# Performance work log

Hardware: AMD Instinct MI355X
Metric: run time of the kernel (lower is better)

The kernel has to match this reference:

```python
import jax, jax.numpy as jnp
import numpy as np

N_POS = 1024
ALPHA = 0.3
B, S = 32, 1024


def setup_inputs() -> dict:
    key = jax.random.key(0)
    k1, k2, k3, k4 = jax.random.split(key, 4)
    s_arc = jax.random.normal(k1, (B, S, S), dtype=jnp.float32)
    a_arc = jax.random.normal(k2, (B, S, S), dtype=jnp.float32)
    adds = jax.random.randint(k3, (B, S), 0, N_POS, dtype=jnp.int32)
    pos = jax.random.randint(k4, (B, S), 0, N_POS, dtype=jnp.int32)
    return {"s_arc": s_arc, "a_arc": a_arc, "adds": adds, "pos": pos}


def reference(s_arc, a_arc, adds, pos):
    n_bins = N_POS * N_POS
    # --- histogram (scatter-add) of a_arc by POS-pair index ---
    # original: _add[b,p1,p2] = adds[b,p1]*seq_len + adds[b,p2]
    sl = adds.shape[1]
    pair_idx = adds[:, :, None] * sl + adds[:, None, :]            # [B,S,S]
    # indices >= n_bins never match any bin in the original masked-sum loop;
    # segment_sum with num_segments=n_bins drops them identically.
    hist = jax.ops.segment_sum(a_arc.reshape(-1), pair_idx.reshape(-1),
                               num_segments=n_bins)                # [n_pos^2]
    score_arc = jax.nn.sigmoid(hist)
    # --- gather score back into s_arc ---
    slp = pos.shape[1]
    pidx = pos[:, :, None] * slp + pos[:, None, :]                  # [B,S,S]
    valid = pidx < n_bins
    gathered = score_arc[jnp.clip(pidx, 0, n_bins - 1)]
    return s_arc + ALPHA * jnp.where(valid, gathered, jnp.float32(0))
```

## Files before the change

### kernel.cpp

```cpp
#include <hip/hip_runtime.h>

#define NPOS 1024
#define BB   32
#define SS   1024
#define ALPHA_C 0.3f
#define CAP  128
#define PAD  1024
#define OCAP 1024
#define MAXO 16
#define PADPAIR 0x04000400u

typedef const __attribute__((address_space(1))) unsigned int guint;
typedef __attribute__((address_space(3))) unsigned int luint;

__global__ __launch_bounds__(256) void zero_fill(float4* __restrict__ p) {
    p[blockIdx.x * 256 + threadIdx.x] = make_float4(0.f, 0.f, 0.f, 0.f);
}

__global__ __launch_bounds__(1024) void build_tables(
    const int* __restrict__ adds, int* __restrict__ cnt, int* __restrict__ list,
    ushort* __restrict__ ell16, int* __restrict__ ocnt, int* __restrict__ oent) {
    __shared__ int scnt[NPOS];
    __shared__ int so;
    const int b = blockIdx.x, t = threadIdx.x;
    const int c = adds[b * SS + t];
    ((uint2*)ell16)[b * 1024 + t] = make_uint2(PADPAIR, PADPAIR);
    scnt[t] = 0;
    if (t == 0) so = 0;
    __syncthreads();
    const int rslot = atomicAdd(&cnt[c], 1);
    if (rslot < CAP) list[c * CAP + rslot] = b * SS + t;
    const int slot = atomicAdd(&scnt[c], 1);
    if (slot < 4) {
        ell16[(((size_t)b * 512 + (c & 511)) * 2 + (c >> 9)) * 4 + slot] = (ushort)t;
    } else {
        const int o = atomicAdd(&so, 1);
        if (o < OCAP) oent[b * OCAP + o] = (c << 10) | t;
    }
    __syncthreads();
    if (t == 0) ocnt[b] = (so < OCAP) ? so : OCAP;
}

__global__ __launch_bounds__(256) void overflow_fixup(
    const float* __restrict__ a, const int* __restrict__ adds,
    const int* __restrict__ ocnt, const int* __restrict__ oent,
    float* __restrict__ hist) {
    const int b  = blockIdx.x;
    const int ei = blockIdx.y;
    if (ei >= ocnt[b]) return;
    const int e  = oent[b * OCAP + ei];
    const int c  = e >> 10, p2 = e & 1023;
    const int p1 = blockIdx.z * 256 + threadIdx.x;
    const int r  = adds[b * SS + p1];
    const float v = a[((size_t)(b * SS + p1)) * SS + p2];
    atomicAdd(&hist[(size_t)r * NPOS + c], v);
}

__global__ __launch_bounds__(512) void hist_rows_kernel(
    const float* __restrict__ a, const int* __restrict__ rowcnt,
    const int* __restrict__ rowlist, const ushort* __restrict__ ell16,
    float* __restrict__ hist) {
    __shared__ float buf[2][NPOS + 2];
    __shared__ int   lsrc[CAP];
    const int r = blockIdx.x, t = threadIdx.x;
    const int w = t >> 6, lane = t & 63;

    int n = rowcnt[r]; if (n > CAP) n = CAP;
    if (t < CAP && t < n) lsrc[t] = rowlist[r * CAP + t];
    if (t == 0) { buf[0][PAD] = 0.f; buf[1][PAD] = 0.f; }
    __syncthreads();

    const uint4* ellv = (const uint4*)ell16;
    float acc0 = 0.f, acc1 = 0.f;
    uint4 E = make_uint4(PADPAIR, PADPAIR, PADPAIR, PADPAIR);

    if (n > 0) {
        if (w < 4) {
            guint* gp = (guint*)(a + (size_t)lsrc[0] * SS + (w << 8) + (lane << 2));
            luint* lp = (luint*)(void*)&buf[0][w << 8];
            __builtin_amdgcn_global_load_lds(gp, lp, 16, 0, 0);
        }
        E = ellv[(size_t)(lsrc[0] >> 10) * 512 + t];
        asm volatile("s_waitcnt vmcnt(0)" ::: "memory");
    }
    __syncthreads();

    for (int k = 0; k < n; ++k) {
        if (k + 1 < n && w < 4) {
            guint* gp = (guint*)(a + (size_t)lsrc[k + 1] * SS + (w << 8) + (lane << 2));
            luint* lp = (luint*)(void*)&buf[(k + 1) & 1][w << 8];
            __builtin_amdgcn_global_load_lds(gp, lp, 16, 0, 0);
        }
        uint4 F = make_uint4(PADPAIR, PADPAIR, PADPAIR, PADPAIR);
        if (k + 1 < n) F = ellv[(size_t)(lsrc[k + 1] >> 10) * 512 + t];

        const float* rb = buf[k & 1];
        acc0 += rb[E.x & 0xffffu]; acc0 += rb[E.x >> 16];
        acc0 += rb[E.y & 0xffffu]; acc0 += rb[E.y >> 16];
        acc1 += rb[E.z & 0xffffu]; acc1 += rb[E.z >> 16];
        acc1 += rb[E.w & 0xffffu]; acc1 += rb[E.w >> 16];
        E = F;

        asm volatile("s_waitcnt vmcnt(0) lgkmcnt(0)" ::: "memory");
        __builtin_amdgcn_s_barrier();
    }

    const size_t o0 = (size_t)r * NPOS + t;
    const float base0 = hist[o0], base1 = hist[o0 + 512];
    hist[o0]       = 1.f / (1.f + __expf(-(base0 + acc0)));
    hist[o0 + 512] = 1.f / (1.f + __expf(-(base1 + acc1)));
}

__global__ __launch_bounds__(256) void gather_kernel(
    const float* __restrict__ s, const int* __restrict__ pos,
    const float* __restrict__ score, float* __restrict__ out) {
    const int row = blockIdx.x;
    const int b   = row >> 10;
    const int*  posb = pos + b * SS;
    const int   base = posb[row & 1023] * NPOS;
    const size_t off = (size_t)row * SS;

    const int t = threadIdx.x;
    float4 v = ((const float4*)(s + off))[t];
    int4   c = ((const int4*)posb)[t];
    float4 o;
    o.x = v.x + ALPHA_C * score[base + c.x];
    o.y = v.y + ALPHA_C * score[base + c.y];
    o.z = v.z + ALPHA_C * score[base + c.z];
    o.w = v.w + ALPHA_C * score[base + c.w];
    ((float4*)(out + off))[t] = o;
}

extern "C" void kernel_launch(void* const* d_in, const int* in_sizes, int n_in,
                              void* d_out, int out_size, void* d_ws, size_t ws_size,
                              hipStream_t stream) {
    const float* s_arc = (const float*)d_in[0];
    const float* a_arc = (const float*)d_in[1];
    const int*   adds  = (const int*)d_in[2];
    const int*   pos   = (const int*)d_in[3];
    float* out  = (float*)d_out;

    float*  hist  = (float*)d_ws;
    int*    cnt   = (int*)((char*)d_ws + (size_t)NPOS * NPOS * sizeof(float));
    int*    list  = cnt + NPOS;
    ushort* ell16 = (ushort*)(list + NPOS * CAP);
    int*    ocnt  = (int*)(ell16 + (size_t)BB * NPOS * 4);
    int*    oent  = ocnt + BB;

    zero_fill<<<1025, 256, 0, stream>>>((float4*)hist);
    build_tables<<<BB, 1024, 0, stream>>>(adds, cnt, list, ell16, ocnt, oent);
    overflow_fixup<<<dim3(BB, MAXO, SS / 256), 256, 0, stream>>>(a_arc, adds, ocnt, oent, hist);
    hist_rows_kernel<<<NPOS, 512, 0, stream>>>(a_arc, cnt, list, ell16, hist);
    gather_kernel<<<BB * SS, 256, 0, stream>>>(s_arc, pos, hist, out);
}
```

Measured before the change: 138.6 us.

## Triple-buffer histogram row loads with prefetch distance two and byte-offset indices

The histogram row kernel moves from a double-buffered LDS ring to a triple-buffered one. Each source row of a_arc is prefetched two iterations ahead, and the per-iteration wait is relaxed from vmcnt(0) to vmcnt(2), so global-to-LDS loads overlap more of the gather-accumulate work. The ELL table now stores byte offsets (t<<2), which drops the index scaling from the inner loop, and the buffer stride is padded. The risk is correctness: the relaxed wait counts and the lack of an explicit lgkmcnt wait depend on the exact order in which loads are issued.

```diff
diff --git a/kernel.cpp b/kernel.cpp
--- a/kernel.cpp
+++ b/kernel.cpp
@@ -5,10 +5,10 @@
 #define SS   1024
 #define ALPHA_C 0.3f
 #define CAP  128
-#define PAD  1024
 #define OCAP 1024
 #define MAXO 16
-#define PADPAIR 0x04000400u
+#define PADPAIR 0x10001000u
+#define BSTRIDE 1032
 
 typedef const __attribute__((address_space(1))) unsigned int guint;
 typedef __attribute__((address_space(3))) unsigned int luint;
@@ -32,7 +32,7 @@
     if (rslot < CAP) list[c * CAP + rslot] = b * SS + t;
     const int slot = atomicAdd(&scnt[c], 1);
     if (slot < 4) {
-        ell16[(((size_t)b * 512 + (c & 511)) * 2 + (c >> 9)) * 4 + slot] = (ushort)t;
+        ell16[(((size_t)b * 512 + (c & 511)) * 2 + (c >> 9)) * 4 + slot] = (ushort)(t << 2);
     } else {
         const int o = atomicAdd(&so, 1);
         if (o < OCAP) oent[b * OCAP + o] = (c << 10) | t;
@@ -60,49 +60,70 @@
     const float* __restrict__ a, const int* __restrict__ rowcnt,
     const int* __restrict__ rowlist, const ushort* __restrict__ ell16,
     float* __restrict__ hist) {
-    __shared__ float buf[2][NPOS + 2];
+    __shared__ float bufflat[3 * BSTRIDE];
     __shared__ int   lsrc[CAP];
     const int r = blockIdx.x, t = threadIdx.x;
     const int w = t >> 6, lane = t & 63;
 
     int n = rowcnt[r]; if (n > CAP) n = CAP;
     if (t < CAP && t < n) lsrc[t] = rowlist[r * CAP + t];
-    if (t == 0) { buf[0][PAD] = 0.f; buf[1][PAD] = 0.f; }
+    if (t < 3) bufflat[t * BSTRIDE + 1024] = 0.f;
     __syncthreads();
 
     const uint4* ellv = (const uint4*)ell16;
     float acc0 = 0.f, acc1 = 0.f;
     uint4 E = make_uint4(PADPAIR, PADPAIR, PADPAIR, PADPAIR);
+    int s1 = 0, s2 = 0;
 
     if (n > 0) {
+        E = ellv[(size_t)(lsrc[0] >> 10) * 512 + t];
         if (w < 4) {
             guint* gp = (guint*)(a + (size_t)lsrc[0] * SS + (w << 8) + (lane << 2));
-            luint* lp = (luint*)(void*)&buf[0][w << 8];
+            luint* lp = (luint*)(void*)&bufflat[0 * BSTRIDE + (w << 8)];
             __builtin_amdgcn_global_load_lds(gp, lp, 16, 0, 0);
         }
-        E = ellv[(size_t)(lsrc[0] >> 10) * 512 + t];
-        asm volatile("s_waitcnt vmcnt(0)" ::: "memory");
+        if (n > 1) {
+            s1 = lsrc[1];
+            if (w < 4) {
+                guint* gp = (guint*)(a + (size_t)s1 * SS + (w << 8) + (lane << 2));
+                luint* lp = (luint*)(void*)&bufflat[1 * BSTRIDE + (w << 8)];
+                __builtin_amdgcn_global_load_lds(gp, lp, 16, 0, 0);
+            }
+        }
+        if (n > 2) s2 = lsrc[2];
     }
-    __syncthreads();
+    asm volatile("s_waitcnt vmcnt(0)" ::: "memory");
+    __builtin_amdgcn_s_barrier();
 
+    int cur = 0;
     for (int k = 0; k < n; ++k) {
-        if (k + 1 < n && w < 4) {
-            guint* gp = (guint*)(a + (size_t)lsrc[k + 1] * SS + (w << 8) + (lane << 2));
-            luint* lp = (luint*)(void*)&buf[(k + 1) & 1][w << 8];
+        int nx = cur + 2; if (nx >= 3) nx -= 3;
+        if (k + 2 < n && w < 4) {
+            guint* gp = (guint*)(a + (size_t)s2 * SS + (w << 8) + (lane << 2));
+            luint* lp = (luint*)(void*)&bufflat[nx * BSTRIDE + (w << 8)];
             __builtin_amdgcn_global_load_lds(gp, lp, 16, 0, 0);
         }
         uint4 F = make_uint4(PADPAIR, PADPAIR, PADPAIR, PADPAIR);
-        if (k + 1 < n) F = ellv[(size_t)(lsrc[k + 1] >> 10) * 512 + t];
+        if (k + 1 < n) F = ellv[(size_t)(s1 >> 10) * 512 + t];
+        __builtin_amdgcn_sched_barrier(0);
 
-        const float* rb = buf[k & 1];
-        acc0 += rb[E.x & 0xffffu]; acc0 += rb[E.x >> 16];
-        acc0 += rb[E.y & 0xffffu]; acc0 += rb[E.y >> 16];
-        acc1 += rb[E.z & 0xffffu]; acc1 += rb[E.z >> 16];
-        acc1 += rb[E.w & 0xffffu]; acc1 += rb[E.w >> 16];
+        const char* rb = (const char*)(bufflat + cur * BSTRIDE);
+        acc0 += *(const float*)(rb + (E.x & 0xffffu));
+        acc0 += *(const float*)(rb + (E.x >> 16));
+        acc0 += *(const float*)(rb + (E.y & 0xffffu));
+        acc0 += *(const float*)(rb + (E.y >> 16));
+        acc1 += *(const float*)(rb + (E.z & 0xffffu));
+        acc1 += *(const float*)(rb + (E.z >> 16));
+        acc1 += *(const float*)(rb + (E.w & 0xffffu));
+        acc1 += *(const float*)(rb + (E.w >> 16));
+        s1 = s2;
+        s2 = (k + 3 < n) ? lsrc[k + 3] : 0;
+        __builtin_amdgcn_sched_barrier(0);
+
+        asm volatile("s_waitcnt vmcnt(2)" ::: "memory");
+        __builtin_amdgcn_s_barrier();
         E = F;
-
-        asm volatile("s_waitcnt vmcnt(0) lgkmcnt(0)" ::: "memory");
-        __builtin_amdgcn_s_barrier();
+        cur = cur + 1; if (cur >= 3) cur -= 3;
     }
 
     const size_t o0 = (size_t)r * NPOS + t;
```

New measurement: 139.7 us. About the same (+0.8%).
